# Performance work log

Measured on AMD Instinct MI355X. Metric: run time of the kernel, lower is better.

Reference implementation:

```python
import jax, jax.numpy as jnp
import numpy as np

QMAX = 127.0  # 8-bit narrow-range symmetric: values in [-127, 127]


def _quantize_per_tensor(t):
    """Symmetric per-tensor int8 quantization (narrow range, like Brevitas Int8*PerTensorFloat).
    Returns (int8 codes as int32 for matmul, float scale)."""
    scale = jnp.max(jnp.abs(t)) / QMAX
    q = jnp.clip(jnp.round(t / scale), -QMAX, QMAX).astype(jnp.int8)
    return q, scale


def setup_inputs() -> dict:
    key = jax.random.key(0)
    k_x, k_w, k_b = jax.random.split(key, 3)
    size_in, size_out, n = 1024, 1024, 32768
    x = jax.random.normal(k_x, (n, size_in), dtype=jnp.float32)
    # kaiming_uniform_(a=sqrt(5)) on [size_out, size_in] -> bound = 1/sqrt(size_in)
    bound = 1.0 / np.sqrt(size_in)
    weight = jax.random.uniform(k_w, (size_out, size_in), dtype=jnp.float32,
                                minval=-bound, maxval=bound)
    bias = jax.random.uniform(k_b, (size_out,), dtype=jnp.float32,
                              minval=-bound, maxval=bound)
    return {"x": x, "weight": weight, "bias": bias}


def reference(x, weight, bias):
    # Quantize activations and weights to int8 per-tensor symmetric.
    qx, sx = _quantize_per_tensor(x)        # [N, K] int8, scalar scale
    qw, sw = _quantize_per_tensor(weight)   # [M, K] int8, scalar scale
    # Approximate-multiplier GEMM modeled as exact int8 MAC with int32 accum
    # (mul8s_acc is the accurate 8-bit multiplier LUT).
    acc = jnp.matmul(qx.astype(jnp.int32), qw.astype(jnp.int32).T)  # [N, M] int32
    # Rescale: output / ((QMAX/input_scale) * (QMAX/weight_scale)) with
    # Brevitas scale conventions == acc * sx * sw here.
    out = acc.astype(jnp.float32) * (sx * sw)
    return out + bias
```

## Files before the change

kernel.cpp:

```cpp
#include <hip/hip_runtime.h>
#include <cstdint>
#include <cstddef>


typedef int v4i __attribute__((ext_vector_type(4)));
typedef int v16i __attribute__((ext_vector_type(16)));

#define QMAXF 127.0f
#define KDIM 1024
#define MDIM 1024
#define NBX 512
#define NBW 32

__global__ __launch_bounds__(256) void absmax_partial(
    const float4* __restrict__ x, int nx4,
    const float4* __restrict__ w, int nw4,
    float* __restrict__ partials) {
  const int b = blockIdx.x;
  const bool isw = (b >= NBX);
  const float4* __restrict__ p = isw ? w : x;
  const int n4 = isw ? nw4 : nx4;
  const int nb = isw ? NBW : NBX;
  const int bb = isw ? (b - NBX) : b;
  const int stride = nb * 256;

  float m0 = 0.f, m1 = 0.f, m2 = 0.f, m3 = 0.f;
  int i = bb * 256 + threadIdx.x;
  for (; i + 3 * stride < n4; i += 4 * stride) {
    float4 v0 = p[i], v1 = p[i + stride], v2 = p[i + 2 * stride],
           v3 = p[i + 3 * stride];
    m0 = fmaxf(m0, fmaxf(fmaxf(fabsf(v0.x), fabsf(v0.y)),
                         fmaxf(fabsf(v0.z), fabsf(v0.w))));
    m1 = fmaxf(m1, fmaxf(fmaxf(fabsf(v1.x), fabsf(v1.y)),
                         fmaxf(fabsf(v1.z), fabsf(v1.w))));
    m2 = fmaxf(m2, fmaxf(fmaxf(fabsf(v2.x), fabsf(v2.y)),
                         fmaxf(fabsf(v2.z), fabsf(v2.w))));
    m3 = fmaxf(m3, fmaxf(fmaxf(fabsf(v3.x), fabsf(v3.y)),
                         fmaxf(fabsf(v3.z), fabsf(v3.w))));
  }
  for (; i < n4; i += stride) {
    float4 v = p[i];
    m0 = fmaxf(m0, fmaxf(fmaxf(fabsf(v.x), fabsf(v.y)),
                         fmaxf(fabsf(v.z), fabsf(v.w))));
  }
  float m = fmaxf(fmaxf(m0, m1), fmaxf(m2, m3));
  for (int off = 32; off; off >>= 1) m = fmaxf(m, __shfl_down(m, off, 64));
  __shared__ float wm[4];
  const int lane = threadIdx.x & 63, wid = threadIdx.x >> 6;
  if (lane == 0) wm[wid] = m;
  __syncthreads();
  if (threadIdx.x == 0)
    partials[b] = fmaxf(fmaxf(wm[0], wm[1]), fmaxf(wm[2], wm[3]));
}

__global__ __launch_bounds__(256) void quant2(
    const float4* __restrict__ x, int nx16,
    const float4* __restrict__ w, int nw16,
    const float* __restrict__ partials,
    v4i* __restrict__ qx, v4i* __restrict__ qw,
    float* __restrict__ amax_out) {
  const int sel = blockIdx.y;
  const float* pp = partials + (sel ? NBX : 0);
  const int np = sel ? NBW : NBX;
  float m = 0.f;
  for (int i = threadIdx.x; i < np; i += 256) m = fmaxf(m, pp[i]);
  for (int off = 32; off; off >>= 1) m = fmaxf(m, __shfl_down(m, off, 64));
  __shared__ float wm[4];
  __shared__ float bmax;
  const int lane = threadIdx.x & 63, wid = threadIdx.x >> 6;
  if (lane == 0) wm[wid] = m;
  __syncthreads();
  if (threadIdx.x == 0) {
    float bm = fmaxf(fmaxf(wm[0], wm[1]), fmaxf(wm[2], wm[3]));
    bmax = bm;
    if (blockIdx.x == 0) amax_out[sel] = bm;
  }
  __syncthreads();
  const float amax = bmax;
  const float r = QMAXF / amax;

  const float4* __restrict__ p = sel ? w : x;
  const int n16 = sel ? nw16 : nx16;
  v4i* __restrict__ q = sel ? qw : qx;

  for (int i = blockIdx.x * 256 + threadIdx.x; i < n16;
       i += gridDim.x * 256) {
    float4 v0 = p[4 * i], v1 = p[4 * i + 1], v2 = p[4 * i + 2],
           v3 = p[4 * i + 3];
    v4i o;
#define QPK(V)                                                         \
  ((((int)fminf(fmaxf(rintf((V).x * r), -QMAXF), QMAXF)) & 255) |      \
   ((((int)fminf(fmaxf(rintf((V).y * r), -QMAXF), QMAXF)) & 255) << 8) | \
   ((((int)fminf(fmaxf(rintf((V).z * r), -QMAXF), QMAXF)) & 255) << 16) | \
   ((((int)fminf(fmaxf(rintf((V).w * r), -QMAXF), QMAXF)) & 255) << 24))
    o[0] = QPK(v0);
    o[1] = QPK(v1);
    o[2] = QPK(v2);
    o[3] = QPK(v3);
#undef QPK
    q[i] = o;
  }
}


__device__ __forceinline__ void ld_lds16(const void* g, void* l) {
  __builtin_amdgcn_global_load_lds(
      (__attribute__((address_space(1))) void*)(void*)g,
      (__attribute__((address_space(3))) void*)l, 16, 0, 0);
}

#define SBAR() asm volatile("s_barrier" ::: "memory")
#define WAITV(n) asm volatile("s_waitcnt vmcnt(" #n ")" ::: "memory")
#define WAITVLG() asm volatile("s_waitcnt vmcnt(0) lgkmcnt(0)" ::: "memory")

#define BK 128
#define BMT 256
#define BNT 256

__global__ __launch_bounds__(512, 2) void gemm_i8(
    const char* __restrict__ qx, const char* __restrict__ qw,
    const float* __restrict__ bias, const float* __restrict__ amax,
    float* __restrict__ out) {
  __shared__ __align__(16) char smA[2][BNT * BK];
  __shared__ __align__(16) char smB[2][BMT * BK];

  const int tid = threadIdx.x;
  const int wave = tid >> 6;
  const int lane = tid & 63;

  const int p = blockIdx.x;
  const int i_ = p >> 3;
  const int bn = (p & 7) * 16 + (i_ >> 2);
  const int bm = i_ & 3;

  const int wn = wave >> 1;
  const int wm = wave & 1;

  const char* __restrict__ xb = qx + (size_t)bn * BNT * KDIM;
  const char* __restrict__ wb = qw + (size_t)bm * BMT * KDIM;

  const int lrow = lane >> 3;
  const int sgx = (lane & 7) ^ lrow;
  const int gcol = sgx * 16;
  const int l31 = lane & 31;
  const int lhi = lane >> 5;

  v16i acc[2][4] = {};

#define STAGE8(bufc, kb) do {                                               \
    _Pragma("unroll") for (int c = 0; c < 4; ++c) {                         \
      const int rb = (wave * 4 + c) * 8;                                    \
      ld_lds16(wb + (size_t)(rb + lrow) * KDIM + (kb) + gcol,               \
               &smB[bufc][rb * BK]);                                        \
    }                                                                       \
    _Pragma("unroll") for (int c = 0; c < 4; ++c) {                         \
      const int rb = (wave * 4 + c) * 8;                                    \
      ld_lds16(xb + (size_t)(rb + lrow) * KDIM + (kb) + gcol,               \
               &smA[bufc][rb * BK]);                                        \
    }                                                                       \
  } while (0)

#define PHASE(bufc, ph, STG, WT) do {                                       \
    v4i a_[2][2], b_[2][4];                                                 \
    _Pragma("unroll") for (int ks = 0; ks < 2; ++ks) {                      \
      const int s = ((ph) * 2 + ks) * 2 + lhi;            \
      _Pragma("unroll") for (int i = 0; i < 2; ++i) {                       \
        const int r = wn * 64 + i * 32 + l31;                               \
        a_[ks][i] = *(const v4i*)(&smA[bufc][r * BK + ((s ^ (r & 7)) * 16)]);\
      }                                                                     \
      _Pragma("unroll") for (int j = 0; j < 4; ++j) {                       \
        const int r = wm * 128 + j * 32 + l31;                              \
        b_[ks][j] = *(const v4i*)(&smB[bufc][r * BK + ((s ^ (r & 7)) * 16)]);\
      }                                                                     \
    }                                                                       \
    STG;                                                                    \
    WT;                                                                     \
    SBAR();                                                                 \
    __builtin_amdgcn_s_setprio(1);                                          \
    _Pragma("unroll") for (int ks = 0; ks < 2; ++ks)                        \
      _Pragma("unroll") for (int i = 0; i < 2; ++i)                         \
        _Pragma("unroll") for (int j = 0; j < 4; ++j)                       \
          acc[i][j] = __builtin_amdgcn_mfma_i32_32x32x32_i8(                \
              a_[ks][i], b_[ks][j], acc[i][j], 0, 0, 0);                    \
    __builtin_amdgcn_s_setprio(0);                                          \
  } while (0)

#define TILE(bufc, kb1)                                                     \
    PHASE(bufc, 0, STAGE8((bufc) ^ 1, kb1), (void)0);                       \
    PHASE(bufc, 1, (void)0, WAITVLG());

  STAGE8(0, 0);
  WAITV(0);
  SBAR();

  TILE(0, 1 * BK);
  TILE(1, 2 * BK);
  TILE(0, 3 * BK);
  TILE(1, 4 * BK);
  TILE(0, 5 * BK);
  TILE(1, 6 * BK);
  TILE(0, 7 * BK);
  PHASE(1, 0, (void)0, (void)0);
  PHASE(1, 1, (void)0, (void)0);

#undef TILE
#undef PHASE
#undef STAGE8

  const float sfac = (amax[0] / QMAXF) * (amax[1] / QMAXF);
  const int mcol = bm * BMT + wm * 128 + l31;
  const int nb0 = bn * BNT + wn * 64 + 4 * lhi;
  float bv[4];
#pragma unroll
  for (int j = 0; j < 4; ++j) bv[j] = bias[mcol + j * 32];
#pragma unroll
  for (int i = 0; i < 2; ++i) {
#pragma unroll
    for (int r = 0; r < 16; ++r) {
      const int n = nb0 + i * 32 + (r & 3) + 8 * (r >> 2);
      float* orow = out + (size_t)n * MDIM + mcol;
#pragma unroll
      for (int j = 0; j < 4; ++j)
        orow[j * 32] = (float)acc[i][j][r] * sfac + bv[j];
    }
  }
}

extern "C" void kernel_launch(void* const* d_in, const int* in_sizes, int n_in,
                              void* d_out, int out_size, void* d_ws, size_t ws_size,
                              hipStream_t stream) {
  const float* x = (const float*)d_in[0];
  const float* w = (const float*)d_in[1];
  const float* bias = (const float*)d_in[2];
  float* out = (float*)d_out;

  const int NX = in_sizes[0];
  const int NW = in_sizes[1];
  const int N = NX / KDIM;

  float* amax = (float*)d_ws;
  float* partials = (float*)((char*)d_ws + 64);
  char* qx = (char*)d_ws + 4096;
  char* qw = qx + (size_t)NX;

  absmax_partial<<<NBX + NBW, 256, 0, stream>>>(
      (const float4*)x, NX / 4, (const float4*)w, NW / 4, partials);

  dim3 qgrid(1024, 2);
  quant2<<<qgrid, 256, 0, stream>>>((const float4*)x, NX / 16,
                                    (const float4*)w, NW / 16, partials,
                                    (v4i*)qx, (v4i*)qw, amax);

  gemm_i8<<<dim3(512), 512, 0, stream>>>(qx, qw, bias, amax, out);
}
```

Before: 292.1 us.

## Shrink GEMM tiles and use triple-buffered LDS pipeline with higher occupancy

The int8 GEMM block tile goes from 256x256 with K-step 128 to 128x256 with K-step 64. The LDS ring becomes three buffers with two stages in flight, using partial vmcnt waits, and the grid doubles to 1024 blocks with launch bounds for four blocks per CU. The aim is to hide global-to-LDS latency better and raise occupancy and load balance. In exchange the smaller per-wave tile (2x2 MFMA) gives less operand reuse, there are more barriers, and the swizzle pattern changes.

Measured after the change: 291.7 us. No clear change (-0.1%).

```diff
diff --git a/kernel.cpp b/kernel.cpp
--- a/kernel.cpp
+++ b/kernel.cpp
@@ -111,18 +111,19 @@
 
 #define SBAR() asm volatile("s_barrier" ::: "memory")
 #define WAITV(n) asm volatile("s_waitcnt vmcnt(" #n ")" ::: "memory")
-#define WAITVLG() asm volatile("s_waitcnt vmcnt(0) lgkmcnt(0)" ::: "memory")
-
-#define BK 128
+#define WAIT_V3_LG() asm volatile("s_waitcnt vmcnt(3) lgkmcnt(0)" ::: "memory")
+#define WAIT_V0_LG() asm volatile("s_waitcnt vmcnt(0) lgkmcnt(0)" ::: "memory")
+
+#define BK 64
+#define BNT 128
 #define BMT 256
-#define BNT 256
-
-__global__ __launch_bounds__(512, 2) void gemm_i8(
+
+__global__ __launch_bounds__(512, 4) void gemm_i8(
     const char* __restrict__ qx, const char* __restrict__ qw,
     const float* __restrict__ bias, const float* __restrict__ amax,
     float* __restrict__ out) {
-  __shared__ __align__(16) char smA[2][BNT * BK];
-  __shared__ __align__(16) char smB[2][BMT * BK];
+  __shared__ __align__(16) char smA[3][BNT * BK];
+  __shared__ __align__(16) char smB[3][BMT * BK];
 
   const int tid = threadIdx.x;
   const int wave = tid >> 6;
@@ -130,97 +131,99 @@
 
   const int p = blockIdx.x;
   const int i_ = p >> 3;
-  const int bn = (p & 7) * 16 + (i_ >> 2);
+  const int bn = (p & 7) * 32 + (i_ >> 2);
   const int bm = i_ & 3;
 
-  const int wn = wave >> 1;
-  const int wm = wave & 1;
+  const int wn = wave >> 2;
+  const int wm = wave & 3;
 
   const char* __restrict__ xb = qx + (size_t)bn * BNT * KDIM;
   const char* __restrict__ wb = qw + (size_t)bm * BMT * KDIM;
 
-  const int lrow = lane >> 3;
-  const int sgx = (lane & 7) ^ lrow;
-  const int gcol = sgx * 16;
+  const int lrow = lane >> 2;
+  const int gseg = ((lane & 3) ^ ((lane >> 3) & 3)) * 16;
   const int l31 = lane & 31;
   const int lhi = lane >> 5;
 
-  v16i acc[2][4] = {};
-
-#define STAGE8(bufc, kb) do {                                               \
-    _Pragma("unroll") for (int c = 0; c < 4; ++c) {                         \
-      const int rb = (wave * 4 + c) * 8;                                    \
-      ld_lds16(wb + (size_t)(rb + lrow) * KDIM + (kb) + gcol,               \
-               &smB[bufc][rb * BK]);                                        \
-    }                                                                       \
-    _Pragma("unroll") for (int c = 0; c < 4; ++c) {                         \
-      const int rb = (wave * 4 + c) * 8;                                    \
-      ld_lds16(xb + (size_t)(rb + lrow) * KDIM + (kb) + gcol,               \
-               &smA[bufc][rb * BK]);                                        \
-    }                                                                       \
+  v16i acc[2][2] = {};
+
+#define STAGE3(bufc, kb) do {                                               \
+    const int ra = wave * 16;                                               \
+    ld_lds16(xb + (size_t)(ra + lrow) * KDIM + (kb) + gseg,                 \
+             &smA[bufc][ra * BK]);                                          \
+    const int rb0 = wave * 32;                                              \
+    ld_lds16(wb + (size_t)(rb0 + lrow) * KDIM + (kb) + gseg,                \
+             &smB[bufc][rb0 * BK]);                                         \
+    ld_lds16(wb + (size_t)(rb0 + 16 + lrow) * KDIM + (kb) + gseg,           \
+             &smB[bufc][(rb0 + 16) * BK]);                                  \
   } while (0)
 
-#define PHASE(bufc, ph, STG, WT) do {                                       \
-    v4i a_[2][2], b_[2][4];                                                 \
+#define PHASE(bufc, STG, WT, BARX) do {                                     \
+    v4i a_[2][2], b_[2][2];                                                 \
     _Pragma("unroll") for (int ks = 0; ks < 2; ++ks) {                      \
-      const int s = ((ph) * 2 + ks) * 2 + lhi;            \
+      const int s = ks * 2 + lhi;                         \
       _Pragma("unroll") for (int i = 0; i < 2; ++i) {                       \
         const int r = wn * 64 + i * 32 + l31;                               \
-        a_[ks][i] = *(const v4i*)(&smA[bufc][r * BK + ((s ^ (r & 7)) * 16)]);\
+        a_[ks][i] = *(const v4i*)(                                          \
+            &smA[bufc][r * BK + ((s ^ ((r >> 1) & 3)) * 16)]);              \
       }                                                                     \
-      _Pragma("unroll") for (int j = 0; j < 4; ++j) {                       \
-        const int r = wm * 128 + j * 32 + l31;                              \
-        b_[ks][j] = *(const v4i*)(&smB[bufc][r * BK + ((s ^ (r & 7)) * 16)]);\
+      _Pragma("unroll") for (int j = 0; j < 2; ++j) {                       \
+        const int r = wm * 64 + j * 32 + l31;                               \
+        b_[ks][j] = *(const v4i*)(                                          \
+            &smB[bufc][r * BK + ((s ^ ((r >> 1) & 3)) * 16)]);              \
       }                                                                     \
     }                                                                       \
     STG;                                                                    \
     WT;                                                                     \
-    SBAR();                                                                 \
+    BARX;                                                                   \
     __builtin_amdgcn_s_setprio(1);                                          \
     _Pragma("unroll") for (int ks = 0; ks < 2; ++ks)                        \
       _Pragma("unroll") for (int i = 0; i < 2; ++i)                         \
-        _Pragma("unroll") for (int j = 0; j < 4; ++j)                       \
+        _Pragma("unroll") for (int j = 0; j < 2; ++j)                       \
           acc[i][j] = __builtin_amdgcn_mfma_i32_32x32x32_i8(                \
               a_[ks][i], b_[ks][j], acc[i][j], 0, 0, 0);                    \
     __builtin_amdgcn_s_setprio(0);                                          \
   } while (0)
 
-#define TILE(bufc, kb1)                                                     \
-    PHASE(bufc, 0, STAGE8((bufc) ^ 1, kb1), (void)0);                       \
-    PHASE(bufc, 1, (void)0, WAITVLG());
-
-  STAGE8(0, 0);
-  WAITV(0);
+  STAGE3(0, 0);
+  STAGE3(1, BK);
+  WAITV(3);
   SBAR();
 
-  TILE(0, 1 * BK);
-  TILE(1, 2 * BK);
-  TILE(0, 3 * BK);
-  TILE(1, 4 * BK);
-  TILE(0, 5 * BK);
-  TILE(1, 6 * BK);
-  TILE(0, 7 * BK);
-  PHASE(1, 0, (void)0, (void)0);
-  PHASE(1, 1, (void)0, (void)0);
-
-#undef TILE
+  PHASE(0, STAGE3(2, 2 * BK), WAIT_V3_LG(), SBAR());
+  PHASE(1, STAGE3(0, 3 * BK), WAIT_V3_LG(), SBAR());
+  PHASE(2, STAGE3(1, 4 * BK), WAIT_V3_LG(), SBAR());
+  PHASE(0, STAGE3(2, 5 * BK), WAIT_V3_LG(), SBAR());
+  PHASE(1, STAGE3(0, 6 * BK), WAIT_V3_LG(), SBAR());
+  PHASE(2, STAGE3(1, 7 * BK), WAIT_V3_LG(), SBAR());
+  PHASE(0, STAGE3(2, 8 * BK), WAIT_V3_LG(), SBAR());
+  PHASE(1, STAGE3(0, 9 * BK), WAIT_V3_LG(), SBAR());
+  PHASE(2, STAGE3(1, 10 * BK), WAIT_V3_LG(), SBAR());
+  PHASE(0, STAGE3(2, 11 * BK), WAIT_V3_LG(), SBAR());
+  PHASE(1, STAGE3(0, 12 * BK), WAIT_V3_LG(), SBAR());
+  PHASE(2, STAGE3(1, 13 * BK), WAIT_V3_LG(), SBAR());
+  PHASE(0, STAGE3(2, 14 * BK), WAIT_V3_LG(), SBAR());
+  PHASE(1, STAGE3(0, 15 * BK), WAIT_V3_LG(), SBAR());
+  PHASE(2, (void)0, WAIT_V0_LG(), SBAR());
+  PHASE(0, (void)0, (void)0, (void)0);
+
 #undef PHASE
-#undef STAGE8
+#undef STAGE3
 
   const float sfac = (amax[0] / QMAXF) * (amax[1] / QMAXF);
-  const int mcol = bm * BMT + wm * 128 + l31;
+  const int mbase = bm * BMT + wm * 64 + l31;
   const int nb0 = bn * BNT + wn * 64 + 4 * lhi;
-  float bv[4];
-#pragma unroll
-  for (int j = 0; j < 4; ++j) bv[j] = bias[mcol + j * 32];
+  float bv[2];
+#pragma unroll
+  for (int j = 0; j < 2; ++j) bv[j] = bias[mbase + j * 32];
 #pragma unroll
   for (int i = 0; i < 2; ++i) {
 #pragma unroll
     for (int r = 0; r < 16; ++r) {
       const int n = nb0 + i * 32 + (r & 3) + 8 * (r >> 2);
-      float* orow = out + (size_t)n * MDIM + mcol;
-#pragma unroll
-      for (int j = 0; j < 4; ++j)
+      float* orow = out + (size_t)n * MDIM + mbase;
+#pragma unroll
+      for (int j = 0; j < 2; ++j)
         orow[j * 32] = (float)acc[i][j][r] * sfac + bv[j];
     }
   }
@@ -251,5 +254,5 @@
                                     (const float4*)w, NW / 16, partials,
                                     (v4i*)qx, (v4i*)qw, amax);
 
-  gemm_i8<<<dim3(512), 512, 0, stream>>>(qx, qw, bias, amax, out);
-}
+  gemm_i8<<<dim3(1024), 512, 0, stream>>>(qx, qw, bias, amax, out);
+}
```
